# Kernel optimization log

Measured on AMD Instinct MI355X. Metric: run time of the kernel, lower is better.

## Reference

```python
import jax, jax.numpy as jnp
import numpy as np

H, KVH, D = 32, 8, 128  # heads, kv heads, head_dim
ROPE_BASE = 10000.0

def _rotate_half(x):
    x1, x2 = x[..., : D // 2], x[..., D // 2 :]
    return jnp.concatenate((-x2, x1), axis=-1)

def _rope_tables(seq_len, dtype):
    inv_freq = 1.0 / (ROPE_BASE ** (jnp.arange(0, D, 2, dtype=jnp.float32) / D))
    t = jnp.arange(seq_len, dtype=jnp.float32)
    freqs = jnp.outer(t, inv_freq)            # [S, D/2]
    emb = jnp.concatenate((freqs, freqs), -1)  # [S, D]
    return jnp.cos(emb).astype(dtype), jnp.sin(emb).astype(dtype)

def setup_inputs() -> dict:
    key = jax.random.key(0)
    ks = jax.random.split(key, 8)
    B, S, E = 2, 2048, 4096
    hidden_states = jax.random.normal(ks[0], (B, S, E), jnp.float32)
    # additive causal mask [B,1,S,S]
    causal = jnp.tril(jnp.ones((S, S), bool))
    attention_mask = jnp.where(causal, 0.0, -1e9).astype(jnp.float32)
    attention_mask = jnp.broadcast_to(attention_mask[None, None], (B, 1, S, S))
    position_ids = jnp.broadcast_to(jnp.arange(S, dtype=jnp.int32)[None], (B, S))
    sd = 0.02
    Wq = jax.random.normal(ks[1], (E, H * D), jnp.float32) * sd
    Wk = jax.random.normal(ks[2], (E, KVH * D), jnp.float32) * sd
    Wv = jax.random.normal(ks[3], (E, KVH * D), jnp.float32) * sd
    Wo = jax.random.normal(ks[4], (H * D, E), jnp.float32) * sd
    bq = jax.random.normal(ks[5], (H * D,), jnp.float32) * sd
    bk = jax.random.normal(ks[6], (KVH * D,), jnp.float32) * sd
    bv = jax.random.normal(ks[7], (KVH * D,), jnp.float32) * sd
    return {"hidden_states": hidden_states, "attention_mask": attention_mask,
            "position_ids": position_ids, "Wq": Wq, "bq": bq, "Wk": Wk, "bk": bk,
            "Wv": Wv, "bv": bv, "Wo": Wo}

def reference(hidden_states, attention_mask, position_ids, Wq, bq, Wk, bk, Wv, bv, Wo):
    B, S, E = hidden_states.shape
    q = (hidden_states @ Wq + bq).reshape(B, S, H, D)
    k = (hidden_states @ Wk + bk).reshape(B, S, KVH, D)
    v = (hidden_states @ Wv + bv).reshape(B, S, KVH, D)
    cos, sin = _rope_tables(S, hidden_states.dtype)
    cos_p = cos[position_ids][:, :, None, :]  # [B,S,1,D]
    sin_p = sin[position_ids][:, :, None, :]
    q = q * cos_p + _rotate_half(q) * sin_p
    k = k * cos_p + _rotate_half(k) * sin_p
    # [B,H,S,D]; expand KV heads for GQA (repeat_interleave along head dim)
    q = q.transpose(0, 2, 1, 3)
    k = jnp.repeat(k.transpose(0, 2, 1, 3), H // KVH, axis=1)
    v = jnp.repeat(v.transpose(0, 2, 1, 3), H // KVH, axis=1)
    scores = jnp.einsum('bhqd,bhkd->bhqk', q, k) / np.sqrt(D).astype(np.float32)
    scores = scores + attention_mask
    attn = jax.nn.softmax(scores.astype(jnp.float32), axis=-1).astype(q.dtype)
    out = jnp.einsum('bhqk,bhkd->bhqd', attn, v)  # [B,H,S,D]
    out = out.transpose(0, 2, 1, 3).reshape(B, S, H * D)
    return out @ Wo
```

## Files before the change

### kernel.cpp

```cpp
#include <hip/hip_runtime.h>

#define B_ 2
#define S_ 2048
#define E_ 4096
#define NH 32
#define NKV 8
#define DH 128

typedef __attribute__((ext_vector_type(8))) short short8;
typedef __attribute__((ext_vector_type(4))) float f32x4;

__device__ __forceinline__ unsigned short f2bf(float f) {
  unsigned int u = __float_as_uint(f);
  u += 0x7fffu + ((u >> 16) & 1u);
  return (unsigned short)(u >> 16);
}
__device__ __forceinline__ float bf2f(unsigned short u) {
  return __uint_as_float(((unsigned int)u) << 16);
}

__device__ __forceinline__ void async16(const void* g, void* l) {
  __builtin_amdgcn_global_load_lds(
      (__attribute__((address_space(1))) void*)const_cast<void*>(g),
      (__attribute__((address_space(3))) void*)l, 16, 0, 0);
}

__global__ void k_cvt(const float4* __restrict__ in, ushort4* __restrict__ out, int n4) {
  int i = blockIdx.x * blockDim.x + threadIdx.x;
  if (i >= n4) return;
  float4 v = in[i];
  ushort4 o;
  o.x = f2bf(v.x); o.y = f2bf(v.y); o.z = f2bf(v.z); o.w = f2bf(v.w);
  out[i] = o;
}

__global__ void k_transpose(const float* __restrict__ in, unsigned short* __restrict__ out,
                            int K, int N) {
  __shared__ float tile[32][33];
  int n0 = blockIdx.x * 32, k0 = blockIdx.y * 32;
  int tx = threadIdx.x, ty = threadIdx.y;
#pragma unroll
  for (int j = 0; j < 32; j += 8)
    tile[ty + j][tx] = in[(size_t)(k0 + ty + j) * N + n0 + tx];
  __syncthreads();
#pragma unroll
  for (int j = 0; j < 32; j += 8)
    out[(size_t)(n0 + ty + j) * K + k0 + tx] = f2bf(tile[tx][ty + j]);
}

__global__ void k_rope(unsigned short* buf, int heads, const int* __restrict__ pos) {
  int i = blockIdx.x * blockDim.x + threadIdx.x;
  int d = i & 63;
  int s = (i >> 6) & (S_ - 1);
  int bh = i >> 17;
  int b = bh / heads;
  float p = (float)pos[b * S_ + s];
  float fr = p * expf(-0.14391156831212787f * (float)d);
  float c, sn;
  sincosf(fr, &sn, &c);
  size_t base = ((size_t)bh * S_ + s) * DH;
  float x1 = bf2f(buf[base + d]);
  float x2 = bf2f(buf[base + d + 64]);
  buf[base + d]      = f2bf(x1 * c - x2 * sn);
  buf[base + d + 64] = f2bf(x2 * c + x1 * sn);
}

template <int MODE>
__global__ __launch_bounds__(256) void k_gemm(
    const unsigned short* __restrict__ A, const unsigned short* __restrict__ Bt, int K,
    const float* __restrict__ bq, const float* __restrict__ bk, const float* __restrict__ bv,
    unsigned short* __restrict__ Qo, unsigned short* __restrict__ Ko,
    unsigned short* __restrict__ Vo, float* __restrict__ Co) {
  __shared__ __align__(16) unsigned short As[2][128 * 64];
  __shared__ __align__(16) unsigned short Bs[2][128 * 64];
  const int tid = threadIdx.x;
  const int wave = tid >> 6, lane = tid & 63;
  const int l15 = lane & 15, quad = lane >> 4;
  const int bid = blockIdx.x;
  const int m0 = (bid & 31) * 128, n0 = (bid >> 5) * 128;
  const int wm = (wave & 1) * 64, wn = (wave >> 1) * 64;

  f32x4 acc[4][4] = {};

  auto stage = [&](int p, int k0) {
#pragma unroll
    for (int j = 0; j < 4; ++j) {
      const int e = j * 256 + tid;
      const int row = e >> 3, sl = e & 7;
      const int gseg = sl ^ (row & 7);
      async16(A + (size_t)(m0 + row) * K + k0 + gseg * 8,
              &As[p][(size_t)(j * 256 + wave * 64) * 8]);
      async16(Bt + (size_t)(n0 + row) * K + k0 + gseg * 8,
              &Bs[p][(size_t)(j * 256 + wave * 64) * 8]);
    }
  };

  stage(0, 0);
  int p = 0;
  for (int k0 = 0; k0 < K; k0 += 64) {
    __syncthreads();
    if (k0 + 64 < K) stage(p ^ 1, k0 + 64);
#pragma unroll
    for (int kk = 0; kk < 2; ++kk) {
      short8 af[4], bfr[4];
#pragma unroll
      for (int i = 0; i < 4; ++i)
        af[i] = *(const short8*)&As[p][(wm + i * 16 + l15) * 64 +
                                       (((kk << 2) + quad) ^ (l15 & 7)) * 8];
#pragma unroll
      for (int i = 0; i < 4; ++i)
        bfr[i] = *(const short8*)&Bs[p][(wn + i * 16 + l15) * 64 +
                                        (((kk << 2) + quad) ^ (l15 & 7)) * 8];
#pragma unroll
      for (int mi = 0; mi < 4; ++mi)
#pragma unroll
        for (int ni = 0; ni < 4; ++ni)
          acc[mi][ni] = __builtin_amdgcn_mfma_f32_16x16x32_bf16(af[mi], bfr[ni], acc[mi][ni], 0, 0, 0);
    }
    p ^= 1;
  }

#pragma unroll
  for (int mi = 0; mi < 4; ++mi) {
#pragma unroll
    for (int ni = 0; ni < 4; ++ni) {
      const int col = n0 + wn + ni * 16 + l15;
      const int rowb = m0 + wm + mi * 16 + quad * 4;
      if constexpr (MODE == 1) {
#pragma unroll
        for (int r = 0; r < 4; ++r)
          Co[(size_t)(rowb + r) * E_ + col] = acc[mi][ni][r];
      } else {
#pragma unroll
        for (int r = 0; r < 4; ++r) {
          const int row = rowb + r;
          const int b = row >> 11, s = row & (S_ - 1);
          float v = acc[mi][ni][r];
          if (col < 4096) {
            v += bq[col];
            const int h = col >> 7, d = col & 127;
            Qo[(((size_t)b * NH + h) * S_ + s) * DH + d] = f2bf(v);
          } else if (col < 5120) {
            const int t = col - 4096;
            v += bk[t];
            const int h = t >> 7, d = t & 127;
            Ko[(((size_t)b * NKV + h) * S_ + s) * DH + d] = f2bf(v);
          } else {
            const int t = col - 5120;
            v += bv[t];
            const int h = t >> 7, d = t & 127;
            Vo[(((size_t)b * NKV + h) * DH + d) * S_ + s] = f2bf(v);
          }
        }
      }
    }
  }
}

__global__ __launch_bounds__(256) void k_attn(
    const unsigned short* __restrict__ Q, const unsigned short* __restrict__ Kb,
    const unsigned short* __restrict__ Vt, unsigned short* __restrict__ O) {
  __shared__ unsigned short Ks[128 * 128];
  __shared__ unsigned short Vs[128 * 128];
  __shared__ unsigned short Ps[64 * 128];
  const int tid = threadIdx.x;
  const int wave = tid >> 6, lane = tid & 63;
  const int l15 = lane & 15, quad = lane >> 4;
  const int bid = blockIdx.x;
  const int qt = bid & 31;
  const int h = (bid >> 5) & 31;
  const int b = bid >> 10;
  const int kvh = h >> 2;
  const int q0 = qt * 64;

  const unsigned short* Qp = Q + ((size_t)b * NH + h) * S_ * DH;
  const unsigned short* Kp = Kb + ((size_t)b * NKV + kvh) * S_ * DH;
  const unsigned short* Vp = Vt + ((size_t)b * NKV + kvh) * DH * (size_t)S_;

  short8 qf[4];
  {
    const unsigned short* qp = Qp + (size_t)(q0 + wave * 16 + l15) * DH + quad * 8;
#pragma unroll
    for (int kk = 0; kk < 4; ++kk) qf[kk] = *(const short8*)(qp + kk * 32);
  }

  f32x4 of[8] = {};
  float mrow[4], lrow[4];
#pragma unroll
  for (int r = 0; r < 4; ++r) { mrow[r] = -1e30f; lrow[r] = 0.f; }

  const int jmax = q0 >> 7;
  const float scale = 0.08838834764831845f;
  unsigned short* Pw = &Ps[wave * 16 * 128];

  for (int j = 0; j <= jmax; ++j) {
    const int kv0 = j * 128;
#pragma unroll
    for (int r = 0; r < 8; ++r) {
      const int e = r * 256 + wave * 64 + lane;
      const int row = e >> 4, slot = e & 15;
      const int gseg = slot ^ (row & 15);
      async16(Kp + (size_t)(kv0 + row) * DH + gseg * 8, &Ks[(size_t)(r * 256 + wave * 64) * 8]);
    }
#pragma unroll
    for (int r = 0; r < 8; ++r) {
      const int e = r * 256 + wave * 64 + lane;
      const int row = e >> 4, slot = e & 15;
      const int gseg = slot ^ (row & 15);
      async16(Vp + (size_t)row * S_ + kv0 + gseg * 8, &Vs[(size_t)(r * 256 + wave * 64) * 8]);
    }
    __syncthreads();

    f32x4 sf[8];
#pragma unroll
    for (int ni = 0; ni < 8; ++ni) {
      f32x4 a = {};
#pragma unroll
      for (int kk = 0; kk < 4; ++kk) {
        const int rowi = ni * 16 + l15;
        short8 kf = *(const short8*)&Ks[rowi * 128 + ((kk * 4 + quad) ^ l15) * 8];
        a = __builtin_amdgcn_mfma_f32_16x16x32_bf16(qf[kk], kf, a, 0, 0, 0);
      }
      sf[ni] = a * scale;
    }

    if (j == jmax) {
#pragma unroll
      for (int ni = 0; ni < 8; ++ni) {
        const int col = kv0 + ni * 16 + l15;
#pragma unroll
        for (int r = 0; r < 4; ++r) {
          const int row = q0 + wave * 16 + quad * 4 + r;
          if (col > row) sf[ni][r] = -1e30f;
        }
      }
    }

#pragma unroll
    for (int r = 0; r < 4; ++r) {
      float cm = sf[0][r];
#pragma unroll
      for (int ni = 1; ni < 8; ++ni) cm = fmaxf(cm, sf[ni][r]);
      cm = fmaxf(cm, __shfl_xor(cm, 1));
      cm = fmaxf(cm, __shfl_xor(cm, 2));
      cm = fmaxf(cm, __shfl_xor(cm, 4));
      cm = fmaxf(cm, __shfl_xor(cm, 8));
      const float nm = fmaxf(mrow[r], cm);
      const float alpha = __expf(mrow[r] - nm);
      mrow[r] = nm;
      float rs = 0.f;
#pragma unroll
      for (int ni = 0; ni < 8; ++ni) {
        const float p = __expf(sf[ni][r] - nm);
        sf[ni][r] = p;
        rs += p;
      }
      rs += __shfl_xor(rs, 1);
      rs += __shfl_xor(rs, 2);
      rs += __shfl_xor(rs, 4);
      rs += __shfl_xor(rs, 8);
      lrow[r] = lrow[r] * alpha + rs;
#pragma unroll
      for (int ni = 0; ni < 8; ++ni) of[ni][r] *= alpha;
    }

#pragma unroll
    for (int ni = 0; ni < 8; ++ni) {
#pragma unroll
      for (int r = 0; r < 4; ++r) {
        const int pr = quad * 4 + r;
        const int c = ni * 16 + l15;
        const int slot = (c >> 3) ^ pr;
        Pw[pr * 128 + slot * 8 + (c & 7)] =
            (unsigned short)(__float_as_uint(sf[ni][r]) >> 16);
      }
    }
    short8 pf[4];
#pragma unroll
    for (int kk = 0; kk < 4; ++kk)
      pf[kk] = *(const short8*)&Pw[l15 * 128 + ((kk * 4 + quad) ^ l15) * 8];

#pragma unroll
    for (int ni = 0; ni < 8; ++ni) {
#pragma unroll
      for (int kk = 0; kk < 4; ++kk) {
        const int rowi = ni * 16 + l15;
        short8 vf = *(const short8*)&Vs[rowi * 128 + ((kk * 4 + quad) ^ l15) * 8];
        of[ni] = __builtin_amdgcn_mfma_f32_16x16x32_bf16(pf[kk], vf, of[ni], 0, 0, 0);
      }
    }
    __syncthreads();
  }

  float il[4];
#pragma unroll
  for (int r = 0; r < 4; ++r) il[r] = 1.0f / lrow[r];
#pragma unroll
  for (int ni = 0; ni < 8; ++ni) {
#pragma unroll
    for (int r = 0; r < 4; ++r) {
      const int row = q0 + wave * 16 + quad * 4 + r;
      const int d = ni * 16 + l15;
      O[(((size_t)b * S_ + row) * NH + h) * DH + d] = f2bf(of[ni][r] * il[r]);
    }
  }
}

extern "C" void kernel_launch(void* const* d_in, const int* in_sizes, int n_in,
                              void* d_out, int out_size, void* d_ws, size_t ws_size,
                              hipStream_t stream) {
  const float* hs = (const float*)d_in[0];
  const int* pos = (const int*)d_in[2];
  const float* Wq = (const float*)d_in[3];
  const float* bq = (const float*)d_in[4];
  const float* Wk = (const float*)d_in[5];
  const float* bk = (const float*)d_in[6];
  const float* Wv = (const float*)d_in[7];
  const float* bv = (const float*)d_in[8];
  const float* Wo = (const float*)d_in[9];
  float* out = (float*)d_out;

  unsigned char* ws = (unsigned char*)d_ws;
  unsigned short* X   = (unsigned short*)(ws);
  unsigned short* WT  = (unsigned short*)(ws + 33554432ull);
  unsigned short* Qb  = (unsigned short*)(ws + 83886080ull);
  unsigned short* Kb  = (unsigned short*)(ws + 117440512ull);
  unsigned short* Vtb = (unsigned short*)(ws + 125829120ull);
  unsigned short* Ob  = X;
  unsigned short* WoT = WT;

  dim3 tb(32, 8);
  k_cvt<<<16384, 256, 0, stream>>>((const float4*)hs, (ushort4*)X, 4194304);
  k_transpose<<<dim3(128, 128), tb, 0, stream>>>(Wq, WT, 4096, 4096);
  k_transpose<<<dim3(32, 128), tb, 0, stream>>>(Wk, WT + 4096ull * 4096ull, 4096, 1024);
  k_transpose<<<dim3(32, 128), tb, 0, stream>>>(Wv, WT + 5120ull * 4096ull, 4096, 1024);
  k_gemm<0><<<32 * 48, 256, 0, stream>>>(X, WT, 4096, bq, bk, bv, Qb, Kb, Vtb, nullptr);
  k_transpose<<<dim3(128, 128), tb, 0, stream>>>(Wo, WoT, 4096, 4096);
  k_rope<<<32768, 256, 0, stream>>>(Qb, NH, pos);
  k_rope<<<8192, 256, 0, stream>>>(Kb, NKV, pos);
  k_attn<<<2048, 256, 0, stream>>>(Qb, Kb, Vtb, Ob);
  k_gemm<1><<<32 * 32, 256, 0, stream>>>(Ob, WoT, 4096,
                                         nullptr, nullptr, nullptr,
                                         nullptr, nullptr, nullptr, out);
}
```

Before: 917.2 us.

## Switch attention to 32x32x16 MFMA with 128-row query tiles

The flash-attention kernel now gives each wave 32 query rows instead of 16 and uses 32x32x16 bf16 MFMA instructions in place of 16x16x32. A block covers 128 query rows, so half as many blocks are launched, and each K/V tile loaded into LDS serves twice as many queries. The P·V product is split into two 64-column phases to keep the per-wave P buffer small. Register pressure rises (16 accumulator rows per lane, eight Q fragments), and the coarser tiles worsen causal load balance across blocks.

```diff
diff --git a/kernel.cpp b/kernel.cpp
--- a/kernel.cpp
+++ b/kernel.cpp
@@ -9,6 +9,7 @@
 
 typedef __attribute__((ext_vector_type(8))) short short8;
 typedef __attribute__((ext_vector_type(4))) float f32x4;
+typedef __attribute__((ext_vector_type(16))) float f32x16;
 
 __device__ __forceinline__ unsigned short f2bf(float f) {
   unsigned int u = __float_as_uint(f);
@@ -162,36 +163,36 @@
     const unsigned short* __restrict__ Vt, unsigned short* __restrict__ O) {
   __shared__ unsigned short Ks[128 * 128];
   __shared__ unsigned short Vs[128 * 128];
-  __shared__ unsigned short Ps[64 * 128];
+  __shared__ unsigned short Ps[4][32 * 64];
   const int tid = threadIdx.x;
   const int wave = tid >> 6, lane = tid & 63;
-  const int l15 = lane & 15, quad = lane >> 4;
+  const int l31 = lane & 31, half = lane >> 5;
   const int bid = blockIdx.x;
-  const int qt = bid & 31;
-  const int h = (bid >> 5) & 31;
-  const int b = bid >> 10;
+  const int qt = bid & 15;
+  const int h = (bid >> 4) & 31;
+  const int b = bid >> 9;
   const int kvh = h >> 2;
-  const int q0 = qt * 64;
+  const int q0 = qt * 128;
 
   const unsigned short* Qp = Q + ((size_t)b * NH + h) * S_ * DH;
   const unsigned short* Kp = Kb + ((size_t)b * NKV + kvh) * S_ * DH;
   const unsigned short* Vp = Vt + ((size_t)b * NKV + kvh) * DH * (size_t)S_;
 
-  short8 qf[4];
+  short8 qf[8];
   {
-    const unsigned short* qp = Qp + (size_t)(q0 + wave * 16 + l15) * DH + quad * 8;
-#pragma unroll
-    for (int kk = 0; kk < 4; ++kk) qf[kk] = *(const short8*)(qp + kk * 32);
-  }
-
-  f32x4 of[8] = {};
-  float mrow[4], lrow[4];
-#pragma unroll
-  for (int r = 0; r < 4; ++r) { mrow[r] = -1e30f; lrow[r] = 0.f; }
-
-  const int jmax = q0 >> 7;
+    const unsigned short* qp = Qp + (size_t)(q0 + wave * 32 + l31) * DH + half * 8;
+#pragma unroll
+    for (int kb = 0; kb < 8; ++kb) qf[kb] = *(const short8*)(qp + kb * 16);
+  }
+
+  f32x16 of[4] = {};
+  float mrow[16], lrow[16];
+#pragma unroll
+  for (int r = 0; r < 16; ++r) { mrow[r] = -1e30f; lrow[r] = 0.f; }
+
+  const int jmax = qt;
   const float scale = 0.08838834764831845f;
-  unsigned short* Pw = &Ps[wave * 16 * 128];
+  unsigned short* Pw = &Ps[wave][0];
 
   for (int j = 0; j <= jmax; ++j) {
     const int kv0 = j * 128;
@@ -211,97 +212,104 @@
     }
     __syncthreads();
 
-    f32x4 sf[8];
-#pragma unroll
-    for (int ni = 0; ni < 8; ++ni) {
-      f32x4 a = {};
-#pragma unroll
-      for (int kk = 0; kk < 4; ++kk) {
-        const int rowi = ni * 16 + l15;
-        short8 kf = *(const short8*)&Ks[rowi * 128 + ((kk * 4 + quad) ^ l15) * 8];
-        a = __builtin_amdgcn_mfma_f32_16x16x32_bf16(qf[kk], kf, a, 0, 0, 0);
-      }
-      sf[ni] = a * scale;
+    f32x16 sf[4];
+#pragma unroll
+    for (int nv = 0; nv < 4; ++nv) {
+      f32x16 a = {};
+      const int krow = nv * 32 + l31;
+      const unsigned short* kbase = &Ks[krow * 128];
+      const int kx = krow & 15;
+#pragma unroll
+      for (int kb = 0; kb < 8; ++kb) {
+        short8 kf = *(const short8*)(kbase + ((kb * 2 + half) ^ kx) * 8);
+        a = __builtin_amdgcn_mfma_f32_32x32x16_bf16(qf[kb], kf, a, 0, 0, 0);
+      }
+      sf[nv] = a * scale;
     }
 
     if (j == jmax) {
 #pragma unroll
-      for (int ni = 0; ni < 8; ++ni) {
-        const int col = kv0 + ni * 16 + l15;
-#pragma unroll
-        for (int r = 0; r < 4; ++r) {
-          const int row = q0 + wave * 16 + quad * 4 + r;
-          if (col > row) sf[ni][r] = -1e30f;
+      for (int nv = 0; nv < 4; ++nv) {
+        const int col = kv0 + nv * 32 + l31;
+#pragma unroll
+        for (int r = 0; r < 16; ++r) {
+          const int rowq = q0 + wave * 32 + (r & 3) + 8 * (r >> 2) + 4 * half;
+          if (col > rowq) sf[nv][r] = -1e30f;
         }
       }
     }
 
 #pragma unroll
-    for (int r = 0; r < 4; ++r) {
-      float cm = sf[0][r];
-#pragma unroll
-      for (int ni = 1; ni < 8; ++ni) cm = fmaxf(cm, sf[ni][r]);
+    for (int r = 0; r < 16; ++r) {
+      float cm = fmaxf(fmaxf(sf[0][r], sf[1][r]), fmaxf(sf[2][r], sf[3][r]));
       cm = fmaxf(cm, __shfl_xor(cm, 1));
       cm = fmaxf(cm, __shfl_xor(cm, 2));
       cm = fmaxf(cm, __shfl_xor(cm, 4));
       cm = fmaxf(cm, __shfl_xor(cm, 8));
+      cm = fmaxf(cm, __shfl_xor(cm, 16));
       const float nm = fmaxf(mrow[r], cm);
       const float alpha = __expf(mrow[r] - nm);
       mrow[r] = nm;
       float rs = 0.f;
 #pragma unroll
-      for (int ni = 0; ni < 8; ++ni) {
-        const float p = __expf(sf[ni][r] - nm);
-        sf[ni][r] = p;
-        rs += p;
+      for (int nv = 0; nv < 4; ++nv) {
+        const float pv = __expf(sf[nv][r] - nm);
+        sf[nv][r] = pv;
+        rs += pv;
       }
       rs += __shfl_xor(rs, 1);
       rs += __shfl_xor(rs, 2);
       rs += __shfl_xor(rs, 4);
       rs += __shfl_xor(rs, 8);
+      rs += __shfl_xor(rs, 16);
       lrow[r] = lrow[r] * alpha + rs;
 #pragma unroll
-      for (int ni = 0; ni < 8; ++ni) of[ni][r] *= alpha;
-    }
-
-#pragma unroll
-    for (int ni = 0; ni < 8; ++ni) {
-#pragma unroll
-      for (int r = 0; r < 4; ++r) {
-        const int pr = quad * 4 + r;
-        const int c = ni * 16 + l15;
-        const int slot = (c >> 3) ^ pr;
-        Pw[pr * 128 + slot * 8 + (c & 7)] =
-            (unsigned short)(__float_as_uint(sf[ni][r]) >> 16);
-      }
-    }
-    short8 pf[4];
-#pragma unroll
-    for (int kk = 0; kk < 4; ++kk)
-      pf[kk] = *(const short8*)&Pw[l15 * 128 + ((kk * 4 + quad) ^ l15) * 8];
-
-#pragma unroll
-    for (int ni = 0; ni < 8; ++ni) {
-#pragma unroll
-      for (int kk = 0; kk < 4; ++kk) {
-        const int rowi = ni * 16 + l15;
-        short8 vf = *(const short8*)&Vs[rowi * 128 + ((kk * 4 + quad) ^ l15) * 8];
-        of[ni] = __builtin_amdgcn_mfma_f32_16x16x32_bf16(pf[kk], vf, of[ni], 0, 0, 0);
+      for (int nd = 0; nd < 4; ++nd) of[nd][r] *= alpha;
+    }
+
+#pragma unroll
+    for (int ph = 0; ph < 2; ++ph) {
+#pragma unroll
+      for (int nvl = 0; nvl < 2; ++nvl) {
+        const int nv = ph * 2 + nvl;
+        const int slot = nvl * 4 + (l31 >> 3);
+        const int ce = l31 & 7;
+#pragma unroll
+        for (int r = 0; r < 16; ++r) {
+          const int rowp = (r & 3) + 8 * (r >> 2) + 4 * half;
+          Pw[rowp * 64 + (slot ^ (rowp & 7)) * 8 + ce] =
+              (unsigned short)(__float_as_uint(sf[nv][r]) >> 16);
+        }
+      }
+      short8 pf[4];
+#pragma unroll
+      for (int kb = 0; kb < 4; ++kb)
+        pf[kb] = *(const short8*)&Pw[l31 * 64 + (((kb * 2 + half) ^ (l31 & 7)) * 8)];
+#pragma unroll
+      for (int nd = 0; nd < 4; ++nd) {
+        const int drow = nd * 32 + l31;
+        const unsigned short* vbase = &Vs[drow * 128];
+        const int vx = drow & 15;
+#pragma unroll
+        for (int kb = 0; kb < 4; ++kb) {
+          short8 vf = *(const short8*)(vbase + (((ph * 8 + kb * 2 + half) ^ vx) * 8));
+          of[nd] = __builtin_amdgcn_mfma_f32_32x32x16_bf16(pf[kb], vf, of[nd], 0, 0, 0);
+        }
       }
     }
     __syncthreads();
   }
 
-  float il[4];
-#pragma unroll
-  for (int r = 0; r < 4; ++r) il[r] = 1.0f / lrow[r];
-#pragma unroll
-  for (int ni = 0; ni < 8; ++ni) {
-#pragma unroll
-    for (int r = 0; r < 4; ++r) {
-      const int row = q0 + wave * 16 + quad * 4 + r;
-      const int d = ni * 16 + l15;
-      O[(((size_t)b * S_ + row) * NH + h) * DH + d] = f2bf(of[ni][r] * il[r]);
+  float il[16];
+#pragma unroll
+  for (int r = 0; r < 16; ++r) il[r] = 1.0f / lrow[r];
+#pragma unroll
+  for (int nd = 0; nd < 4; ++nd) {
+#pragma unroll
+    for (int r = 0; r < 16; ++r) {
+      const int rowq = q0 + wave * 32 + (r & 3) + 8 * (r >> 2) + 4 * half;
+      const int d = nd * 32 + l31;
+      O[(((size_t)b * S_ + rowq) * NH + h) * DH + d] = f2bf(of[nd][r] * il[r]);
     }
   }
 }
@@ -338,7 +346,7 @@
   k_transpose<<<dim3(128, 128), tb, 0, stream>>>(Wo, WoT, 4096, 4096);
   k_rope<<<32768, 256, 0, stream>>>(Qb, NH, pos);
   k_rope<<<8192, 256, 0, stream>>>(Kb, NKV, pos);
-  k_attn<<<2048, 256, 0, stream>>>(Qb, Kb, Vtb, Ob);
+  k_attn<<<1024, 256, 0, stream>>>(Qb, Kb, Vtb, Ob);
   k_gemm<1><<<32 * 32, 256, 0, stream>>>(Ob, WoT, 4096,
                                          nullptr, nullptr, nullptr,
                                          nullptr, nullptr, nullptr, out);
```

Measured after the change: 1.098 ms. 19.7% more time.

## Double attention query tile to 128 rows per block for K/V reuse

Applied to the files above, without the earlier changes.

The attention kernel now processes 128 query rows per block (32 per wave, two 16-row MFMA sub-tiles) instead of 64, halving the grid size. Each K/V tile loaded into LDS is reused by twice as many queries, cutting global K/V traffic and per-tile sync overhead. The P buffer is restructured into per-wave 32x64 halves processed in two phases to fit LDS. The cost is higher register pressure (two sets of accumulators and softmax state), lower occupancy, and coarser causal load balance with fewer blocks.

```diff
diff --git a/kernel.cpp b/kernel.cpp
--- a/kernel.cpp
+++ b/kernel.cpp
@@ -162,36 +162,40 @@
     const unsigned short* __restrict__ Vt, unsigned short* __restrict__ O) {
   __shared__ unsigned short Ks[128 * 128];
   __shared__ unsigned short Vs[128 * 128];
-  __shared__ unsigned short Ps[64 * 128];
+  __shared__ unsigned short Ps[4][32 * 64];
   const int tid = threadIdx.x;
   const int wave = tid >> 6, lane = tid & 63;
   const int l15 = lane & 15, quad = lane >> 4;
   const int bid = blockIdx.x;
-  const int qt = bid & 31;
-  const int h = (bid >> 5) & 31;
-  const int b = bid >> 10;
+  const int qt = bid & 15;
+  const int h = (bid >> 4) & 31;
+  const int b = bid >> 9;
   const int kvh = h >> 2;
-  const int q0 = qt * 64;
+  const int q0 = qt * 128;
 
   const unsigned short* Qp = Q + ((size_t)b * NH + h) * S_ * DH;
   const unsigned short* Kp = Kb + ((size_t)b * NKV + kvh) * S_ * DH;
   const unsigned short* Vp = Vt + ((size_t)b * NKV + kvh) * DH * (size_t)S_;
 
-  short8 qf[4];
-  {
-    const unsigned short* qp = Qp + (size_t)(q0 + wave * 16 + l15) * DH + quad * 8;
-#pragma unroll
-    for (int kk = 0; kk < 4; ++kk) qf[kk] = *(const short8*)(qp + kk * 32);
+  short8 qf[2][4];
+#pragma unroll
+  for (int mb = 0; mb < 2; ++mb) {
+    const unsigned short* qp =
+        Qp + (size_t)(q0 + wave * 32 + mb * 16 + l15) * DH + quad * 8;
+#pragma unroll
+    for (int kk = 0; kk < 4; ++kk) qf[mb][kk] = *(const short8*)(qp + kk * 32);
   }
 
-  f32x4 of[8] = {};
-  float mrow[4], lrow[4];
-#pragma unroll
-  for (int r = 0; r < 4; ++r) { mrow[r] = -1e30f; lrow[r] = 0.f; }
-
-  const int jmax = q0 >> 7;
+  f32x4 of[2][8] = {};
+  float mrow[2][4], lrow[2][4];
+#pragma unroll
+  for (int mb = 0; mb < 2; ++mb)
+#pragma unroll
+    for (int r = 0; r < 4; ++r) { mrow[mb][r] = -1e30f; lrow[mb][r] = 0.f; }
+
+  const int jmax = qt;
   const float scale = 0.08838834764831845f;
-  unsigned short* Pw = &Ps[wave * 16 * 128];
+  unsigned short* Pw = &Ps[wave][0];
 
   for (int j = 0; j <= jmax; ++j) {
     const int kv0 = j * 128;
@@ -211,99 +215,122 @@
     }
     __syncthreads();
 
-    f32x4 sf[8];
+    f32x4 sf[2][8];
 #pragma unroll
     for (int ni = 0; ni < 8; ++ni) {
-      f32x4 a = {};
+      f32x4 a0 = {}, a1 = {};
+      const int rowi = ni * 16 + l15;
+      const unsigned short* kbase = &Ks[rowi * 128];
 #pragma unroll
       for (int kk = 0; kk < 4; ++kk) {
-        const int rowi = ni * 16 + l15;
-        short8 kf = *(const short8*)&Ks[rowi * 128 + ((kk * 4 + quad) ^ l15) * 8];
-        a = __builtin_amdgcn_mfma_f32_16x16x32_bf16(qf[kk], kf, a, 0, 0, 0);
-      }
-      sf[ni] = a * scale;
+        short8 kf = *(const short8*)(kbase + ((kk * 4 + quad) ^ l15) * 8);
+        a0 = __builtin_amdgcn_mfma_f32_16x16x32_bf16(qf[0][kk], kf, a0, 0, 0, 0);
+        a1 = __builtin_amdgcn_mfma_f32_16x16x32_bf16(qf[1][kk], kf, a1, 0, 0, 0);
+      }
+      sf[0][ni] = a0 * scale;
+      sf[1][ni] = a1 * scale;
     }
 
     if (j == jmax) {
 #pragma unroll
-      for (int ni = 0; ni < 8; ++ni) {
-        const int col = kv0 + ni * 16 + l15;
-#pragma unroll
-        for (int r = 0; r < 4; ++r) {
-          const int row = q0 + wave * 16 + quad * 4 + r;
-          if (col > row) sf[ni][r] = -1e30f;
-        }
-      }
-    }
-
-#pragma unroll
-    for (int r = 0; r < 4; ++r) {
-      float cm = sf[0][r];
-#pragma unroll
-      for (int ni = 1; ni < 8; ++ni) cm = fmaxf(cm, sf[ni][r]);
-      cm = fmaxf(cm, __shfl_xor(cm, 1));
-      cm = fmaxf(cm, __shfl_xor(cm, 2));
-      cm = fmaxf(cm, __shfl_xor(cm, 4));
-      cm = fmaxf(cm, __shfl_xor(cm, 8));
-      const float nm = fmaxf(mrow[r], cm);
-      const float alpha = __expf(mrow[r] - nm);
-      mrow[r] = nm;
-      float rs = 0.f;
-#pragma unroll
-      for (int ni = 0; ni < 8; ++ni) {
-        const float p = __expf(sf[ni][r] - nm);
-        sf[ni][r] = p;
-        rs += p;
-      }
-      rs += __shfl_xor(rs, 1);
-      rs += __shfl_xor(rs, 2);
-      rs += __shfl_xor(rs, 4);
-      rs += __shfl_xor(rs, 8);
-      lrow[r] = lrow[r] * alpha + rs;
-#pragma unroll
-      for (int ni = 0; ni < 8; ++ni) of[ni][r] *= alpha;
-    }
-
-#pragma unroll
-    for (int ni = 0; ni < 8; ++ni) {
+      for (int mb = 0; mb < 2; ++mb)
+#pragma unroll
+        for (int ni = 0; ni < 8; ++ni) {
+          const int col = kv0 + ni * 16 + l15;
+#pragma unroll
+          for (int r = 0; r < 4; ++r) {
+            const int row = q0 + wave * 32 + mb * 16 + quad * 4 + r;
+            if (col > row) sf[mb][ni][r] = -1e30f;
+          }
+        }
+    }
+
+#pragma unroll
+    for (int mb = 0; mb < 2; ++mb)
 #pragma unroll
       for (int r = 0; r < 4; ++r) {
-        const int pr = quad * 4 + r;
-        const int c = ni * 16 + l15;
-        const int slot = (c >> 3) ^ pr;
-        Pw[pr * 128 + slot * 8 + (c & 7)] =
-            (unsigned short)(__float_as_uint(sf[ni][r]) >> 16);
-      }
-    }
-    short8 pf[4];
-#pragma unroll
-    for (int kk = 0; kk < 4; ++kk)
-      pf[kk] = *(const short8*)&Pw[l15 * 128 + ((kk * 4 + quad) ^ l15) * 8];
-
-#pragma unroll
-    for (int ni = 0; ni < 8; ++ni) {
-#pragma unroll
-      for (int kk = 0; kk < 4; ++kk) {
-        const int rowi = ni * 16 + l15;
-        short8 vf = *(const short8*)&Vs[rowi * 128 + ((kk * 4 + quad) ^ l15) * 8];
-        of[ni] = __builtin_amdgcn_mfma_f32_16x16x32_bf16(pf[kk], vf, of[ni], 0, 0, 0);
+        float cm = sf[mb][0][r];
+#pragma unroll
+        for (int ni = 1; ni < 8; ++ni) cm = fmaxf(cm, sf[mb][ni][r]);
+        cm = fmaxf(cm, __shfl_xor(cm, 1));
+        cm = fmaxf(cm, __shfl_xor(cm, 2));
+        cm = fmaxf(cm, __shfl_xor(cm, 4));
+        cm = fmaxf(cm, __shfl_xor(cm, 8));
+        const float nm = fmaxf(mrow[mb][r], cm);
+        const float alpha = __expf(mrow[mb][r] - nm);
+        mrow[mb][r] = nm;
+        float rs = 0.f;
+#pragma unroll
+        for (int ni = 0; ni < 8; ++ni) {
+          const float pv = __expf(sf[mb][ni][r] - nm);
+          sf[mb][ni][r] = pv;
+          rs += pv;
+        }
+        rs += __shfl_xor(rs, 1);
+        rs += __shfl_xor(rs, 2);
+        rs += __shfl_xor(rs, 4);
+        rs += __shfl_xor(rs, 8);
+        lrow[mb][r] = lrow[mb][r] * alpha + rs;
+#pragma unroll
+        for (int ni = 0; ni < 8; ++ni) of[mb][ni][r] *= alpha;
+      }
+
+#pragma unroll
+    for (int ph = 0; ph < 2; ++ph) {
+#pragma unroll
+      for (int mb = 0; mb < 2; ++mb)
+#pragma unroll
+        for (int nl = 0; nl < 4; ++nl) {
+          const int ni = ph * 4 + nl;
+          const int sbase = nl * 2 + (l15 >> 3);
+          const int ce = l15 & 7;
+#pragma unroll
+          for (int r = 0; r < 4; ++r) {
+            const int rowp = mb * 16 + quad * 4 + r;
+            Pw[rowp * 64 + ((sbase ^ (rowp & 7)) * 8) + ce] =
+                (unsigned short)(__float_as_uint(sf[mb][ni][r]) >> 16);
+          }
+        }
+      short8 pfm[2][2];
+#pragma unroll
+      for (int mb = 0; mb < 2; ++mb)
+#pragma unroll
+        for (int k2 = 0; k2 < 2; ++k2) {
+          const int rr = mb * 16 + l15;
+          pfm[mb][k2] =
+              *(const short8*)&Pw[rr * 64 + (((k2 * 4 + quad) ^ (rr & 7)) * 8)];
+        }
+#pragma unroll
+      for (int nd = 0; nd < 8; ++nd) {
+        const int drow = nd * 16 + l15;
+        const unsigned short* vbase = &Vs[drow * 128];
+#pragma unroll
+        for (int k2 = 0; k2 < 2; ++k2) {
+          short8 vf = *(const short8*)(vbase + (((ph * 8 + k2 * 4 + quad) ^ l15) * 8));
+          of[0][nd] = __builtin_amdgcn_mfma_f32_16x16x32_bf16(pfm[0][k2], vf, of[0][nd], 0, 0, 0);
+          of[1][nd] = __builtin_amdgcn_mfma_f32_16x16x32_bf16(pfm[1][k2], vf, of[1][nd], 0, 0, 0);
+        }
       }
     }
     __syncthreads();
   }
 
-  float il[4];
-#pragma unroll
-  for (int r = 0; r < 4; ++r) il[r] = 1.0f / lrow[r];
-#pragma unroll
-  for (int ni = 0; ni < 8; ++ni) {
-#pragma unroll
-    for (int r = 0; r < 4; ++r) {
-      const int row = q0 + wave * 16 + quad * 4 + r;
-      const int d = ni * 16 + l15;
-      O[(((size_t)b * S_ + row) * NH + h) * DH + d] = f2bf(of[ni][r] * il[r]);
-    }
-  }
+  float il[2][4];
+#pragma unroll
+  for (int mb = 0; mb < 2; ++mb)
+#pragma unroll
+    for (int r = 0; r < 4; ++r) il[mb][r] = 1.0f / lrow[mb][r];
+#pragma unroll
+  for (int mb = 0; mb < 2; ++mb)
+#pragma unroll
+    for (int nd = 0; nd < 8; ++nd) {
+#pragma unroll
+      for (int r = 0; r < 4; ++r) {
+        const int row = q0 + wave * 32 + mb * 16 + quad * 4 + r;
+        const int d = nd * 16 + l15;
+        O[(((size_t)b * S_ + row) * NH + h) * DH + d] = f2bf(of[mb][nd][r] * il[mb][r]);
+      }
+    }
 }
 
 extern "C" void kernel_launch(void* const* d_in, const int* in_sizes, int n_in,
@@ -338,7 +365,7 @@
   k_transpose<<<dim3(128, 128), tb, 0, stream>>>(Wo, WoT, 4096, 4096);
   k_rope<<<32768, 256, 0, stream>>>(Qb, NH, pos);
   k_rope<<<8192, 256, 0, stream>>>(Kb, NKV, pos);
-  k_attn<<<2048, 256, 0, stream>>>(Qb, Kb, Vtb, Ob);
+  k_attn<<<1024, 256, 0, stream>>>(Qb, Kb, Vtb, Ob);
   k_gemm<1><<<32 * 32, 256, 0, stream>>>(Ob, WoT, 4096,
                                          nullptr, nullptr, nullptr,
                                          nullptr, nullptr, nullptr, out);
```

After: 1.046 ms. 14.1% more time.
